# Kernel optimization log

Measured on AMD Instinct MI355X. Metric: run time of the kernel, lower is better.

Reference implementation:

```python
import jax, jax.numpy as jnp
import numpy as np

NUM_HEADS = 16
HIDDEN = 1024
TOTAL = 2048
NSEG = 8


def setup_inputs() -> dict:
    key = jax.random.key(0)
    ks = jax.random.split(key, 10)
    x = jax.random.normal(ks[0], (TOTAL, HIDDEN), dtype=jnp.float32)
    # cu_seqlens: [0, b1, ..., TOTAL], sorted segment boundaries
    inner = np.sort(np.random.default_rng(0).integers(1, TOTAL, size=NSEG - 1))
    cu_seqlens = jnp.asarray(np.concatenate([[0], inner, [TOTAL]]), dtype=jnp.int32)
    s = 1.0 / np.sqrt(HIDDEN)
    def lin(k):
        kw, kb = jax.random.split(k)
        W = jax.random.uniform(kw, (HIDDEN, HIDDEN), jnp.float32, -s, s)
        b = jax.random.uniform(kb, (HIDDEN,), jnp.float32, -s, s)
        return W, b
    Wq, bq = lin(ks[1]); Wk, bk = lin(ks[2]); Wv, bv = lin(ks[3]); Wo, bo = lin(ks[4])
    return {"hidden_states_packed": x, "cu_seqlens": cu_seqlens,
            "Wq": Wq, "bq": bq, "Wk": Wk, "bk": bk,
            "Wv": Wv, "bv": bv, "Wo": Wo, "bo": bo}


def reference(hidden_states_packed, cu_seqlens, Wq, bq, Wk, bk, Wv, bv, Wo, bo):
    T, H = hidden_states_packed.shape
    dh = H // NUM_HEADS
    x = hidden_states_packed
    q = (x @ Wq.T + bq).reshape(T, NUM_HEADS, dh)
    k = (x @ Wk.T + bk).reshape(T, NUM_HEADS, dh)
    v = (x @ Wv.T + bv).reshape(T, NUM_HEADS, dh)
    # segment id of each token from cu_seqlens boundaries
    seg = jnp.searchsorted(cu_seqlens, jnp.arange(T, dtype=jnp.int32), side="right")
    same_seg = seg[:, None] == seg[None, :]  # [T, T] block-diagonal mask
    scale = 1.0 / jnp.sqrt(jnp.asarray(dh, x.dtype))
    scores = jnp.einsum("qhd,khd->hqk", q, k) * scale  # [H, T, T]
    neg = jnp.asarray(jnp.finfo(scores.dtype).min, scores.dtype)
    scores = jnp.where(same_seg[None, :, :], scores, neg)
    attn = jax.nn.softmax(scores, axis=-1)
    ctx = jnp.einsum("hqk,khd->qhd", attn, v).reshape(T, H)
    return ctx @ Wo.T + bo
```

## Files before the change

### kernel.cpp

```cpp
#include <hip/hip_runtime.h>

typedef _Float16 f16x8 __attribute__((ext_vector_type(8)));
typedef _Float16 f16x4 __attribute__((ext_vector_type(4)));
typedef float    f32x4 __attribute__((ext_vector_type(4)));

#define MFMA_F16(a, b, c) __builtin_amdgcn_mfma_f32_16x16x32_f16((a), (b), (c), 0, 0, 0)

typedef __attribute__((address_space(1))) void gas_void;
typedef __attribute__((address_space(3))) void las_void;
#define GLOAD_LDS16(g, l) \
  __builtin_amdgcn_global_load_lds((gas_void*)(g), (las_void*)(l), 16, 0, 0)

#define NEG_INF (-__builtin_inff())

constexpr int T_SEQ  = 2048;
constexpr int HID    = 1024;
constexpr int NHEADS = 16;
constexpr int DH     = 64;
constexpr int NSEG   = 8;

__global__ __launch_bounds__(256) void convert_all(
    const float* __restrict__ x,
    const float* __restrict__ Wq, const float* __restrict__ Wk,
    const float* __restrict__ Wv, const float* __restrict__ Wo,
    _Float16* __restrict__ xh,
    _Float16* __restrict__ Wqh, _Float16* __restrict__ Wkh,
    _Float16* __restrict__ Wvh, _Float16* __restrict__ Woh) {
  int i = blockIdx.x * 256 + threadIdx.x;
  const float* src;
  _Float16* dst;
  int local;
  if (i < 524288) {
    src = x; dst = xh; local = i;
  } else {
    int j = i - 524288;
    int w = j >> 18;
    local = j & 262143;
    src = (w == 0) ? Wq : (w == 1) ? Wk : (w == 2) ? Wv : Wo;
    dst = (w == 0) ? Wqh : (w == 1) ? Wkh : (w == 2) ? Wvh : Woh;
  }
  float4 f = *(const float4*)(src + (size_t)local * 4);
  f16x4 h;
  h[0] = (_Float16)f.x; h[1] = (_Float16)f.y;
  h[2] = (_Float16)f.z; h[3] = (_Float16)f.w;
  *(f16x4*)(dst + (size_t)local * 4) = h;
}

template <int LAYOUT>
__device__ __forceinline__ void gemm128(const _Float16* __restrict__ A,
                                        const _Float16* __restrict__ B,
                                        const float* __restrict__ bias,
                                        _Float16* __restrict__ outh,
                                        float* __restrict__ outf) {
  constexpr int K = HID, N = HID;
  __shared__ _Float16 As[128 * 64];
  __shared__ _Float16 Bs[128 * 64];
  const int tid  = threadIdx.x;
  const int wave = tid >> 6, lane = tid & 63;
  const int lr = lane & 15, lq = lane >> 4;
  const int wm = (wave >> 1) * 64, wn = (wave & 1) * 64;
  const int bm = blockIdx.y * 128, bn = blockIdx.x * 128;

  const _Float16* gA[4];
  const _Float16* gB[4];
  _Float16* lA[4];
  _Float16* lB[4];
#pragma unroll
  for (int i = 0; i < 4; ++i) {
    const int s = i * 256 + wave * 64 + lane;
    const int row = s >> 3, pch = s & 7;
    const int lch = pch ^ (row & 7);
    gA[i] = A + (size_t)(bm + row) * K + lch * 8;
    gB[i] = B + (size_t)(bn + row) * K + lch * 8;
    lA[i] = &As[(i * 256 + wave * 64) * 8];
    lB[i] = &Bs[(i * 256 + wave * 64) * 8];
  }

  f32x4 acc[4][4] = {};

  for (int kk = 0; kk < K; kk += 64) {
#pragma unroll
    for (int i = 0; i < 4; ++i) GLOAD_LDS16(gA[i] + kk, lA[i]);
#pragma unroll
    for (int i = 0; i < 4; ++i) GLOAD_LDS16(gB[i] + kk, lB[i]);
    __syncthreads();
#pragma unroll
    for (int ks = 0; ks < 2; ++ks) {
      f16x8 af[4], bf[4];
#pragma unroll
      for (int mi = 0; mi < 4; ++mi) {
        const int row = wm + mi * 16 + lr;
        af[mi] = *(const f16x8*)&As[row * 64 + (((ks * 4 + lq) ^ (row & 7)) * 8)];
      }
#pragma unroll
      for (int ni = 0; ni < 4; ++ni) {
        const int row = wn + ni * 16 + lr;
        bf[ni] = *(const f16x8*)&Bs[row * 64 + (((ks * 4 + lq) ^ (row & 7)) * 8)];
      }
#pragma unroll
      for (int mi = 0; mi < 4; ++mi)
#pragma unroll
        for (int ni = 0; ni < 4; ++ni)
          acc[mi][ni] = MFMA_F16(af[mi], bf[ni], acc[mi][ni]);
    }
    __syncthreads();
  }

#pragma unroll
  for (int ni = 0; ni < 4; ++ni) {
    const int col = bn + wn + ni * 16 + lr;
    const float bv = bias[col];
#pragma unroll
    for (int mi = 0; mi < 4; ++mi) {
      const f32x4 v = acc[mi][ni];
      const int row0 = bm + wm + mi * 16 + lq * 4;
      if (LAYOUT == 3) {
        f16x4 o;
#pragma unroll
        for (int r = 0; r < 4; ++r) o[r] = (_Float16)(v[r] + bv);
        *(f16x4*)&outh[(size_t)col * T_SEQ + row0] = o;
      } else {
#pragma unroll
        for (int r = 0; r < 4; ++r) {
          const int row = row0 + r;
          const float val = v[r] + bv;
          if (LAYOUT == 0)
            outh[((size_t)(col >> 6) * T_SEQ + row) * DH + (col & 63)] = (_Float16)val;
          else
            outf[(size_t)row * N + col] = val;
        }
      }
    }
  }
}

__global__ __launch_bounds__(256) void gemm_qkv(
    const _Float16* __restrict__ xh,
    const _Float16* __restrict__ Wqh, const _Float16* __restrict__ Wkh,
    const _Float16* __restrict__ Wvh,
    const float* __restrict__ bq, const float* __restrict__ bk,
    const float* __restrict__ bv,
    _Float16* __restrict__ qp, _Float16* __restrict__ kp,
    _Float16* __restrict__ vT) {
  const int z = blockIdx.z;
  if (z == 0) {
    gemm128<0>(xh, Wqh, bq, qp, nullptr);
  } else if (z == 1) {
    gemm128<0>(xh, Wkh, bk, kp, nullptr);
  } else {
    gemm128<3>(xh, Wvh, bv, vT, nullptr);
  }
}

__global__ __launch_bounds__(256) void gemm_out(
    const _Float16* __restrict__ ctxh, const _Float16* __restrict__ Woh,
    const float* __restrict__ bo, float* __restrict__ out) {
  gemm128<1>(ctxh, Woh, bo, nullptr, out);
}

__device__ __forceinline__ float redmax16(float v) {
  v = fmaxf(v, __shfl_xor(v, 1));
  v = fmaxf(v, __shfl_xor(v, 2));
  v = fmaxf(v, __shfl_xor(v, 4));
  v = fmaxf(v, __shfl_xor(v, 8));
  return v;
}
__device__ __forceinline__ float redsum16(float v) {
  v += __shfl_xor(v, 1);
  v += __shfl_xor(v, 2);
  v += __shfl_xor(v, 4);
  v += __shfl_xor(v, 8);
  return v;
}

__global__ __launch_bounds__(256, 2) void attn_kernel(
    const _Float16* __restrict__ qp, const _Float16* __restrict__ kp,
    const _Float16* __restrict__ vT, const int* __restrict__ cu,
    _Float16* __restrict__ ctx) {
  constexpr float SCL2E = 0.125f * 1.44269504f;
  constexpr int PSTR = 72;
  __shared__ _Float16 Pl[4 * 16 * PSTR];
  const int h  = blockIdx.y;
  const int q0 = blockIdx.x * 64;
  const int tid = threadIdx.x, wave = tid >> 6, lane = tid & 63;
  const int lr = lane & 15, lq = lane >> 4;
  const int qw = q0 + wave * 16;

  int cs[NSEG + 1];
#pragma unroll
  for (int i = 0; i <= NSEG; ++i) cs[i] = cu[i];

  int sstart[4], send[4];
#pragma unroll
  for (int r = 0; r < 4; ++r) {
    const int row = qw + lq * 4 + r;
    sstart[r] = 0; send[r] = T_SEQ;
#pragma unroll
    for (int s = 0; s < NSEG; ++s)
      if (row >= cs[s] && row < cs[s + 1]) { sstart[r] = cs[s]; send[r] = cs[s + 1]; }
  }
  int klo = 0, khi = T_SEQ;
#pragma unroll
  for (int s = 0; s < NSEG; ++s) {
    if (qw >= cs[s] && qw < cs[s + 1]) klo = cs[s];
    if (qw + 15 >= cs[s] && qw + 15 < cs[s + 1]) khi = cs[s + 1];
  }
  klo &= ~63;

  const _Float16* qbase = qp + ((size_t)h * T_SEQ + qw + lr) * DH;
  const f16x8 qf0 = *(const f16x8*)(qbase + lq * 8);
  const f16x8 qf1 = *(const f16x8*)(qbase + 32 + lq * 8);

  const _Float16* kb = kp + (size_t)h * T_SEQ * DH;
  const _Float16* vb = vT + (size_t)h * DH * T_SEQ;

  float mst[4], lst[4], alpha[4];
  f32x4 oacc[4];
#pragma unroll
  for (int r = 0; r < 4; ++r) { mst[r] = NEG_INF; lst[r] = 0.f; }
#pragma unroll
  for (int c = 0; c < 4; ++c) oacc[c] = f32x4{0.f, 0.f, 0.f, 0.f};

  _Float16* pw = &Pl[wave * 16 * PSTR];

  auto loadK = [&](int kt, f16x8 (&kf)[4][2]) {
#pragma unroll
    for (int n = 0; n < 4; ++n) {
      int row = kt + n * 16 + lr;
      row = (row < T_SEQ - 1) ? row : (T_SEQ - 1);
      const _Float16* p = kb + (size_t)row * DH + lq * 8;
      kf[n][0] = *(const f16x8*)p;
      kf[n][1] = *(const f16x8*)(p + 32);
    }
  };
  auto loadV = [&](int kt, f16x8 (&vf)[4][2]) {
#pragma unroll
    for (int c = 0; c < 4; ++c) {
      const _Float16* p = vb + (size_t)(c * 16 + lr) * T_SEQ + kt + lq * 8;
      vf[c][0] = *(const f16x8*)p;
      vf[c][1] = *(const f16x8*)(p + 32);
    }
  };

  auto step = [&](int kt, f16x8 (&kf)[4][2], f16x8 (&vf)[4][2]) {
    f32x4 sc[4];
#pragma unroll
    for (int n = 0; n < 4; ++n) {
      sc[n] = f32x4{0.f, 0.f, 0.f, 0.f};
      sc[n] = MFMA_F16(qf0, kf[n][0], sc[n]);
      sc[n] = MFMA_F16(qf1, kf[n][1], sc[n]);
    }
#pragma unroll
    for (int r = 0; r < 4; ++r) {
      float vv[4];
#pragma unroll
      for (int n = 0; n < 4; ++n) {
        const int col = kt + n * 16 + lr;
        vv[n] = (col >= sstart[r] && col < send[r]) ? sc[n][r] * SCL2E : NEG_INF;
      }
      float mx = redmax16(fmaxf(fmaxf(vv[0], vv[1]), fmaxf(vv[2], vv[3])));
      const float mnew = fmaxf(mst[r], mx);
      const float msafe = (mnew == NEG_INF) ? 0.f : mnew;
      const float a = (mst[r] == NEG_INF) ? 0.f : exp2f(mst[r] - mnew);
      float p0 = exp2f(vv[0] - msafe);
      float p1 = exp2f(vv[1] - msafe);
      float p2 = exp2f(vv[2] - msafe);
      float p3 = exp2f(vv[3] - msafe);
      const float rs = redsum16((p0 + p1) + (p2 + p3));
      lst[r] = lst[r] * a + rs;
      mst[r] = mnew;
      alpha[r] = a;
      _Float16* pr = &pw[(lq * 4 + r) * PSTR + lr];
      pr[0]  = (_Float16)p0;
      pr[16] = (_Float16)p1;
      pr[32] = (_Float16)p2;
      pr[48] = (_Float16)p3;
    }
#pragma unroll
    for (int c = 0; c < 4; ++c) {
      f32x4 t = oacc[c];
#pragma unroll
      for (int r = 0; r < 4; ++r) t[r] *= alpha[r];
      oacc[c] = t;
    }
    const f16x8 pf0 = *(const f16x8*)&pw[lr * PSTR + lq * 8];
    const f16x8 pf1 = *(const f16x8*)&pw[lr * PSTR + 32 + lq * 8];
#pragma unroll
    for (int c = 0; c < 4; ++c) {
      oacc[c] = MFMA_F16(pf0, vf[c][0], oacc[c]);
      oacc[c] = MFMA_F16(pf1, vf[c][1], oacc[c]);
    }
  };

  f16x8 kA[4][2], vA[4][2], kB[4][2], vB[4][2];
  int kt = klo;
  loadK(kt, kA);
  loadV(kt, vA);
  while (true) {
    if (kt + 64 < khi) { loadK(kt + 64, kB); loadV(kt + 64, vB); }
    step(kt, kA, vA);
    kt += 64;
    if (kt >= khi) break;
    if (kt + 64 < khi) { loadK(kt + 64, kA); loadV(kt + 64, vA); }
    step(kt, kB, vB);
    kt += 64;
    if (kt >= khi) break;
  }

#pragma unroll
  for (int c = 0; c < 4; ++c)
#pragma unroll
    for (int r = 0; r < 4; ++r) {
      const int row = qw + lq * 4 + r;
      ctx[(size_t)row * HID + h * DH + c * 16 + lr] =
          (_Float16)(oacc[c][r] / lst[r]);
    }
}

extern "C" void kernel_launch(void* const* d_in, const int* in_sizes, int n_in,
                              void* d_out, int out_size, void* d_ws, size_t ws_size,
                              hipStream_t stream) {
  const float* x  = (const float*)d_in[0];
  const int* cu   = (const int*)d_in[1];
  const float* Wq = (const float*)d_in[2]; const float* bq = (const float*)d_in[3];
  const float* Wk = (const float*)d_in[4]; const float* bk = (const float*)d_in[5];
  const float* Wv = (const float*)d_in[6]; const float* bv = (const float*)d_in[7];
  const float* Wo = (const float*)d_in[8]; const float* bo = (const float*)d_in[9];
  float* out = (float*)d_out;

  char* ws = (char*)d_ws;
  _Float16* xh   = (_Float16*)(ws + (size_t)0);
  _Float16* Wqh  = (_Float16*)(ws + ((size_t)4 << 20));
  _Float16* Wkh  = (_Float16*)(ws + ((size_t)6 << 20));
  _Float16* Wvh  = (_Float16*)(ws + ((size_t)8 << 20));
  _Float16* Woh  = (_Float16*)(ws + ((size_t)10 << 20));
  _Float16* qp   = (_Float16*)(ws + ((size_t)12 << 20));
  _Float16* kp   = (_Float16*)(ws + ((size_t)16 << 20));
  _Float16* vT   = (_Float16*)(ws + ((size_t)20 << 20));
  _Float16* ctxh = (_Float16*)(ws + ((size_t)24 << 20));

  convert_all<<<6144, 256, 0, stream>>>(x, Wq, Wk, Wv, Wo, xh, Wqh, Wkh, Wvh, Woh);
  gemm_qkv<<<dim3(8, 16, 3), 256, 0, stream>>>(xh, Wqh, Wkh, Wvh, bq, bk, bv, qp, kp, vT);
  attn_kernel<<<dim3(T_SEQ / 64, NHEADS), 256, 0, stream>>>(qp, kp, vT, cu, ctxh);
  gemm_out<<<dim3(8, 16, 1), 256, 0, stream>>>(ctxh, Woh, bo, out);
}
```

Before: 164.1 us.

## Use 8-wave GEMM blocks and 64-row tiles for the output projection

Restructures the shared GEMM helper to run 512 threads (8 waves arranged 2x4), with each wave computing a smaller MI x 2 MFMA tile, and makes the M tile size a template parameter. The QKV GEMM keeps 128x128 tiles, now with more waves per block. The output projection switches to 64x128 tiles, doubling its grid to 256 blocks to fill more compute units. The aim is more parallelism and better latency hiding, at the cost of less reuse of A/B fragments per wave and more LDS reads per MFMA.

```diff
diff --git a/kernel.cpp b/kernel.cpp
--- a/kernel.cpp
+++ b/kernel.cpp
@@ -46,72 +46,81 @@
   *(f16x4*)(dst + (size_t)local * 4) = h;
 }
 
-template <int LAYOUT>
+template <int LAYOUT, int BM>
 __device__ __forceinline__ void gemm128(const _Float16* __restrict__ A,
                                         const _Float16* __restrict__ B,
                                         const float* __restrict__ bias,
                                         _Float16* __restrict__ outh,
                                         float* __restrict__ outf) {
   constexpr int K = HID, N = HID;
-  __shared__ _Float16 As[128 * 64];
+  constexpr int MI = BM / 32;
+  constexpr int LA = (BM * 8) / 512;
+  __shared__ _Float16 As[BM * 64];
   __shared__ _Float16 Bs[128 * 64];
   const int tid  = threadIdx.x;
   const int wave = tid >> 6, lane = tid & 63;
   const int lr = lane & 15, lq = lane >> 4;
-  const int wm = (wave >> 1) * 64, wn = (wave & 1) * 64;
-  const int bm = blockIdx.y * 128, bn = blockIdx.x * 128;
-
-  const _Float16* gA[4];
-  const _Float16* gB[4];
-  _Float16* lA[4];
-  _Float16* lB[4];
-#pragma unroll
-  for (int i = 0; i < 4; ++i) {
-    const int s = i * 256 + wave * 64 + lane;
+  const int wm = (wave >> 2) * (BM / 2);
+  const int wn = (wave & 3) * 32;
+  const int bm = blockIdx.y * BM, bn = blockIdx.x * 128;
+
+  const _Float16* gA[LA > 0 ? LA : 1];
+  const _Float16* gB[2];
+  _Float16* lA[LA > 0 ? LA : 1];
+  _Float16* lB[2];
+#pragma unroll
+  for (int i = 0; i < LA; ++i) {
+    const int s = i * 512 + tid;
     const int row = s >> 3, pch = s & 7;
     const int lch = pch ^ (row & 7);
     gA[i] = A + (size_t)(bm + row) * K + lch * 8;
+    lA[i] = &As[(i * 512 + wave * 64) * 8];
+  }
+#pragma unroll
+  for (int i = 0; i < 2; ++i) {
+    const int s = i * 512 + tid;
+    const int row = s >> 3, pch = s & 7;
+    const int lch = pch ^ (row & 7);
     gB[i] = B + (size_t)(bn + row) * K + lch * 8;
-    lA[i] = &As[(i * 256 + wave * 64) * 8];
-    lB[i] = &Bs[(i * 256 + wave * 64) * 8];
-  }
-
-  f32x4 acc[4][4] = {};
+    lB[i] = &Bs[(i * 512 + wave * 64) * 8];
+  }
+
+  f32x4 acc[MI][2] = {};
 
   for (int kk = 0; kk < K; kk += 64) {
 #pragma unroll
-    for (int i = 0; i < 4; ++i) GLOAD_LDS16(gA[i] + kk, lA[i]);
-#pragma unroll
-    for (int i = 0; i < 4; ++i) GLOAD_LDS16(gB[i] + kk, lB[i]);
+    for (int i = 0; i < LA; ++i) GLOAD_LDS16(gA[i] + kk, lA[i]);
+#pragma unroll
+    for (int i = 0; i < 2; ++i) GLOAD_LDS16(gB[i] + kk, lB[i]);
     __syncthreads();
 #pragma unroll
     for (int ks = 0; ks < 2; ++ks) {
-      f16x8 af[4], bf[4];
-#pragma unroll
-      for (int mi = 0; mi < 4; ++mi) {
+      f16x8 af[MI], bf[2];
+#pragma unroll
+      for (int mi = 0; mi < MI; ++mi) {
         const int row = wm + mi * 16 + lr;
         af[mi] = *(const f16x8*)&As[row * 64 + (((ks * 4 + lq) ^ (row & 7)) * 8)];
       }
 #pragma unroll
-      for (int ni = 0; ni < 4; ++ni) {
+      for (int ni = 0; ni < 2; ++ni) {
         const int row = wn + ni * 16 + lr;
         bf[ni] = *(const f16x8*)&Bs[row * 64 + (((ks * 4 + lq) ^ (row & 7)) * 8)];
       }
 #pragma unroll
-      for (int mi = 0; mi < 4; ++mi)
-#pragma unroll
-        for (int ni = 0; ni < 4; ++ni)
+      for (int mi = 0; mi < MI; ++mi)
+#pragma unroll
+        for (int ni = 0; ni < 2; ++ni)
           acc[mi][ni] = MFMA_F16(af[mi], bf[ni], acc[mi][ni]);
     }
     __syncthreads();
   }
 
 #pragma unroll
-  for (int ni = 0; ni < 4; ++ni) {
+  for (int ni = 0; ni < 2; ++ni) {
     const int col = bn + wn + ni * 16 + lr;
     const float bv = bias[col];
 #pragma unroll
-    for (int mi = 0; mi < 4; ++mi) {
+    for (int mi = 0; mi < MI; ++mi) {
       const f32x4 v = acc[mi][ni];
       const int row0 = bm + wm + mi * 16 + lq * 4;
       if (LAYOUT == 3) {
@@ -134,7 +143,7 @@
   }
 }
 
-__global__ __launch_bounds__(256) void gemm_qkv(
+__global__ __launch_bounds__(512) void gemm_qkv(
     const _Float16* __restrict__ xh,
     const _Float16* __restrict__ Wqh, const _Float16* __restrict__ Wkh,
     const _Float16* __restrict__ Wvh,
@@ -144,18 +153,18 @@
     _Float16* __restrict__ vT) {
   const int z = blockIdx.z;
   if (z == 0) {
-    gemm128<0>(xh, Wqh, bq, qp, nullptr);
+    gemm128<0, 128>(xh, Wqh, bq, qp, nullptr);
   } else if (z == 1) {
-    gemm128<0>(xh, Wkh, bk, kp, nullptr);
+    gemm128<0, 128>(xh, Wkh, bk, kp, nullptr);
   } else {
-    gemm128<3>(xh, Wvh, bv, vT, nullptr);
-  }
-}
-
-__global__ __launch_bounds__(256) void gemm_out(
+    gemm128<3, 128>(xh, Wvh, bv, vT, nullptr);
+  }
+}
+
+__global__ __launch_bounds__(512) void gemm_out(
     const _Float16* __restrict__ ctxh, const _Float16* __restrict__ Woh,
     const float* __restrict__ bo, float* __restrict__ out) {
-  gemm128<1>(ctxh, Woh, bo, nullptr, out);
+  gemm128<1, 64>(ctxh, Woh, bo, nullptr, out);
 }
 
 __device__ __forceinline__ float redmax16(float v) {
@@ -340,7 +349,7 @@
   _Float16* ctxh = (_Float16*)(ws + ((size_t)24 << 20));
 
   convert_all<<<6144, 256, 0, stream>>>(x, Wq, Wk, Wv, Wo, xh, Wqh, Wkh, Wvh, Woh);
-  gemm_qkv<<<dim3(8, 16, 3), 256, 0, stream>>>(xh, Wqh, Wkh, Wvh, bq, bk, bv, qp, kp, vT);
+  gemm_qkv<<<dim3(8, 16, 3), 512, 0, stream>>>(xh, Wqh, Wkh, Wvh, bq, bk, bv, qp, kp, vT);
   attn_kernel<<<dim3(T_SEQ / 64, NHEADS), 256, 0, stream>>>(qp, kp, vT, cu, ctxh);
-  gemm_out<<<dim3(8, 16, 1), 256, 0, stream>>>(ctxh, Woh, bo, out);
-}
+  gemm_out<<<dim3(8, 32), 512, 0, stream>>>(ctxh, Woh, bo, out);
+}
```

New measurement: 158.9 us. -3.2%, faster.
